# Kernel tuning notes

Measured on AMD Instinct MI355X. Metric: run time of the kernel, lower is better.

The kernel has to match this reference:

```python
import jax, jax.numpy as jnp
import numpy as np

V = 128          # vocab_size
S = 32           # sentence_size
E = 16           # embedding_size
M = 128          # memory_size
L = 128          # linear_output_size
B = 16
N = 127


def _position_encoding(sentence_size, embedding_size):
    enc = np.ones((embedding_size, sentence_size), dtype=np.float32)
    ls = sentence_size + 1
    le = embedding_size + 1
    for i in range(1, le):
        for j in range(1, ls):
            enc[i - 1, j - 1] = (i - (le - 1) / 2) * (j - (ls - 1) / 2)
    enc = 1 + 4 * enc / embedding_size / sentence_size
    return enc.T  # [S, E]


def setup_inputs() -> dict:
    key = jax.random.key(0)
    ks = jax.random.split(key, 12)
    node_fts = jax.random.randint(ks[0], (B, N, S), 0, V).astype(jnp.float32)
    edge_fts = jax.random.randint(ks[1], (B, N, N, S), 0, V).astype(jnp.float32)
    graph_fts = jax.random.randint(ks[2], (B, S), 0, V).astype(jnp.float32)
    adj_mat = jax.random.randint(ks[3], (B, N, N), 0, 2).astype(jnp.float32)
    hidden = jnp.zeros((B, N, E), jnp.float32)
    sc = 0.02
    query_biases = sc * jax.random.normal(ks[4], (V - 1, E), jnp.float32)
    stories_biases = sc * jax.random.normal(ks[5], (V - 1, E), jnp.float32)
    output_biases = sc * jax.random.normal(ks[6], (V - 1, E), jnp.float32)
    memory_contents = sc * jax.random.normal(ks[7], (M, E), jnp.float32)
    W_int = sc * jax.random.normal(ks[8], (E, E), jnp.float32)   # intermediate_linear (unused, num_hops=1)
    W_out = sc * jax.random.normal(ks[9], (E, L), jnp.float32)   # output_linear
    W_fin = sc * jax.random.normal(ks[10], (L, V), jnp.float32)  # final_linear
    enc = jnp.asarray(_position_encoding(S, E))
    return dict(node_fts=node_fts, edge_fts=edge_fts, graph_fts=graph_fts,
                adj_mat=adj_mat, hidden=hidden, enc=enc,
                query_biases=query_biases, stories_biases=stories_biases,
                output_biases=output_biases, memory_contents=memory_contents,
                W_int=W_int, W_out=W_out, W_fin=W_fin)


def reference(node_fts, edge_fts, graph_fts, adj_mat, hidden, enc,
              query_biases, stories_biases, output_biases, memory_contents,
              W_int, W_out, W_fin):
    del hidden
    b, n, s = node_fts.shape
    # [B, N+1, S]: nodes plus graph feature row
    naf = jnp.concatenate([node_fts, graph_fts[:, None, :]], axis=1)
    # mask edges then pad to [B, N+1, N+1, S]
    ef = edge_fts * adj_mat[..., None]
    ef = jnp.pad(ef, ((0, 0), (0, 1), (0, 1), (0, 0)))
    bt = b * (n + 1)
    queries = naf.reshape(bt, s)                 # [BT, S]
    stories = ef.reshape(bt, n + 1, s)           # [BT, M0, S], M0 = N+1

    nil = jnp.zeros((1, enc.shape[1]), queries.dtype)
    sb = jnp.concatenate([stories_biases, nil], axis=0)   # [V, E]
    qb = jnp.concatenate([query_biases, nil], axis=0)
    ob = jnp.concatenate([output_biases, nil], axis=0)

    sidx = jnp.maximum(stories.astype(jnp.int32), 0)       # clamp_min(0)
    qidx = jnp.maximum(queries.astype(jnp.int32), 0)

    # position-encoded weighted sums over the sentence axis
    mem = jnp.einsum('bmse,se->bme', sb[sidx], enc)        # [BT, M0, E]
    Cj = jnp.einsum('bmse,se->bme', ob[sidx], enc)         # [BT, M0, E]
    pad_m = memory_contents.shape[0] - (n + 1)
    mem = jnp.pad(mem, ((0, 0), (0, pad_m), (0, 0))) + memory_contents
    Cj = jnp.pad(Cj, ((0, 0), (0, pad_m), (0, 0)))
    u = jnp.einsum('bse,se->be', qb[qidx], enc)            # [BT, E]

    # num_hops = 1
    x = u
    probs = jax.nn.softmax(jnp.einsum('bme,be->bm', mem, x), axis=-1)
    o = jnp.einsum('bme,bm->be', Cj, probs)
    x = jax.nn.relu((x + o) @ W_out)                       # last hop -> output_linear + relu
    ret = x @ W_fin                                        # [BT, V]

    nxt = ret.reshape(b, n + 1, -1)
    return nxt[:, :-1, :] + nxt[:, -1:, :]                 # [B, N, V]
```

## Files before the change

kernel.cpp:

```cpp
#include <hip/hip_runtime.h>

#define Vn 128
#define Bn 16
#define Nn 127
#define BTn 2048
#define RS 20

__global__ __launch_bounds__(256, 4) void memnet_main(
    const float* __restrict__ node_fts, const float* __restrict__ edge_fts,
    const float* __restrict__ graph_fts, const float* __restrict__ adjm,
    const float* __restrict__ enc, const float* __restrict__ qb,
    const float* __restrict__ sb, const float* __restrict__ ob,
    const float* __restrict__ mc, const float* __restrict__ wout,
    const float* __restrict__ wfin, float* __restrict__ ret)
{
    __shared__ __align__(16) float sbL[128 * RS];
    __shared__ __align__(16) float obL[128 * RS];
    __shared__ __align__(16) float encL[32 * 16];
    __shared__ unsigned int idxw[128 * 8];
    __shared__ float cjT[16 * 129];
    __shared__ float scoresL[128];
    __shared__ float probsL[128];
    __shared__ float opart[128];
    __shared__ unsigned char actF[128];
    __shared__ __align__(16) float uL[16];
    __shared__ float uoL[16];
    __shared__ __align__(16) float cCL[16];
    __shared__ float xL[128];
    __shared__ float red[8];
    __shared__ float k0L;

    const int t = threadIdx.x;
    const int bt = blockIdx.x;
    const int b = bt >> 7;
    const int i = bt & 127;

    for (int c = t; c < 512; c += 256) {
        int r = c >> 2, q = c & 3;
        float4 v = make_float4(0.f, 0.f, 0.f, 0.f);
        float4 w = make_float4(0.f, 0.f, 0.f, 0.f);
        if (r < 127) {
            v = *(const float4*)&sb[r * 16 + q * 4];
            w = *(const float4*)&ob[r * 16 + q * 4];
        }
        *(float4*)&sbL[r * RS + q * 4] = v;
        *(float4*)&obL[r * RS + q * 4] = w;
    }
    if (t < 128) {
        *(float4*)&encL[t * 4] = *(const float4*)&enc[t * 4];
    }
    if (t < 128) {
        bool a = false;
        if (t < 127 && i < 127) a = (adjm[(b * 127 + i) * 127 + t] != 0.f);
        actF[t] = a ? 1 : 0;
    }
    for (int c = t; c < 1024; c += 256) {
        int m = c >> 3, q = c & 7;
        unsigned int packed = 0u;
        if (i < 127 && m < 127) {
            float a = adjm[(b * 127 + i) * 127 + m];
            if (a != 0.f) {
                const float4 v = *(const float4*)&edge_fts[(size_t)(((b * 127 + i) * 127 + m)) * 32 + q * 4];
                packed = (unsigned)(int)v.x | ((unsigned)(int)v.y << 8)
                       | ((unsigned)(int)v.z << 16) | ((unsigned)(int)v.w << 24);
            }
        }
        idxw[m * 8 + q] = packed;
    }
    if (t < 16) {
        float es = 0.f;
        for (int s = 0; s < 32; s++) es += enc[s * 16 + t];
        float ue = 0.f;
        for (int s = 0; s < 32; s++) {
            float qv = (i < 127) ? node_fts[(b * 127 + i) * 32 + s] : graph_fts[b * 32 + s];
            int qi = (int)qv;
            if (qi < 0) qi = 0;
            float w = (qi < 127) ? qb[qi * 16 + t] : 0.f;
            ue = fmaf(w, enc[s * 16 + t], ue);
        }
        uL[t] = ue;
        cCL[t] = ob[t] * es;
        float kv = sb[t] * es * ue;
        kv += __shfl_xor(kv, 1); kv += __shfl_xor(kv, 2);
        kv += __shfl_xor(kv, 4); kv += __shfl_xor(kv, 8);
        if (t == 0) k0L = kv;
    }
    __syncthreads();

    const int eg4 = (t & 3) * 4;
    const int md = t >> 2;
    const int m0 = md;
    const int m1 = md + 64;
    const bool a0 = (actF[m0] != 0);
    const bool a1 = (actF[m1] != 0);

    float4 aM0 = make_float4(0.f, 0.f, 0.f, 0.f);
    float4 aM1 = make_float4(0.f, 0.f, 0.f, 0.f);
    float4 aC0 = make_float4(0.f, 0.f, 0.f, 0.f);
    float4 aC1 = make_float4(0.f, 0.f, 0.f, 0.f);

    if (a0) {
#pragma unroll
        for (int sq = 0; sq < 8; sq++) {
            unsigned w0 = idxw[m0 * 8 + sq];
#pragma unroll
            for (int j = 0; j < 4; j++) {
                int s = sq * 4 + j;
                int i0 = (int)((w0 >> (8 * j)) & 0xFF);
                float4 eb = *(const float4*)&encL[s * 16 + eg4];
                float4 a  = *(const float4*)&sbL[i0 * RS + eg4];
                float4 c  = *(const float4*)&obL[i0 * RS + eg4];
                aM0.x = fmaf(a.x, eb.x, aM0.x); aM0.y = fmaf(a.y, eb.y, aM0.y);
                aM0.z = fmaf(a.z, eb.z, aM0.z); aM0.w = fmaf(a.w, eb.w, aM0.w);
                aC0.x = fmaf(c.x, eb.x, aC0.x); aC0.y = fmaf(c.y, eb.y, aC0.y);
                aC0.z = fmaf(c.z, eb.z, aC0.z); aC0.w = fmaf(c.w, eb.w, aC0.w);
            }
        }
    }
    if (a1) {
#pragma unroll
        for (int sq = 0; sq < 8; sq++) {
            unsigned w1 = idxw[m1 * 8 + sq];
#pragma unroll
            for (int j = 0; j < 4; j++) {
                int s = sq * 4 + j;
                int i1 = (int)((w1 >> (8 * j)) & 0xFF);
                float4 eb = *(const float4*)&encL[s * 16 + eg4];
                float4 a  = *(const float4*)&sbL[i1 * RS + eg4];
                float4 c  = *(const float4*)&obL[i1 * RS + eg4];
                aM1.x = fmaf(a.x, eb.x, aM1.x); aM1.y = fmaf(a.y, eb.y, aM1.y);
                aM1.z = fmaf(a.z, eb.z, aM1.z); aM1.w = fmaf(a.w, eb.w, aM1.w);
                aC1.x = fmaf(c.x, eb.x, aC1.x); aC1.y = fmaf(c.y, eb.y, aC1.y);
                aC1.z = fmaf(c.z, eb.z, aC1.z); aC1.w = fmaf(c.w, eb.w, aC1.w);
            }
        }
    }

    {
        float4 u4 = *(const float4*)&uL[eg4];
        float4 mc0 = *(const float4*)&mc[m0 * 16 + eg4];
        float4 mc1 = *(const float4*)&mc[m1 * 16 + eg4];
        float p0 = (aM0.x + mc0.x) * u4.x + (aM0.y + mc0.y) * u4.y
                 + (aM0.z + mc0.z) * u4.z + (aM0.w + mc0.w) * u4.w;
        float p1 = (aM1.x + mc1.x) * u4.x + (aM1.y + mc1.y) * u4.y
                 + (aM1.z + mc1.z) * u4.z + (aM1.w + mc1.w) * u4.w;
        p0 += __shfl_xor(p0, 1); p0 += __shfl_xor(p0, 2);
        p1 += __shfl_xor(p1, 1); p1 += __shfl_xor(p1, 2);
        if ((t & 3) == 0) {
            scoresL[m0] = p0 + (a0 ? 0.f : k0L);
            scoresL[m1] = p1 + (a1 ? 0.f : k0L);
        }
        float4 cC4 = *(const float4*)&cCL[eg4];
        float4 c0 = a0 ? aC0 : cC4;
        float4 c1 = a1 ? aC1 : cC4;
        cjT[(eg4 + 0) * 129 + m0] = c0.x; cjT[(eg4 + 1) * 129 + m0] = c0.y;
        cjT[(eg4 + 2) * 129 + m0] = c0.z; cjT[(eg4 + 3) * 129 + m0] = c0.w;
        cjT[(eg4 + 0) * 129 + m1] = c1.x; cjT[(eg4 + 1) * 129 + m1] = c1.y;
        cjT[(eg4 + 2) * 129 + m1] = c1.z; cjT[(eg4 + 3) * 129 + m1] = c1.w;
    }
    __syncthreads();

    {
        float v = (t < 128) ? scoresL[t] : -1e30f;
#pragma unroll
        for (int off = 32; off > 0; off >>= 1) v = fmaxf(v, __shfl_xor(v, off));
        if ((t & 63) == 0) red[t >> 6] = v;
        __syncthreads();
        float mx = fmaxf(fmaxf(red[0], red[1]), fmaxf(red[2], red[3]));
        float ex = (t < 128) ? __expf(scoresL[t] - mx) : 0.f;
        float sv = ex;
#pragma unroll
        for (int off = 32; off > 0; off >>= 1) sv += __shfl_xor(sv, off);
        __syncthreads();
        if ((t & 63) == 0) red[t >> 6] = sv;
        __syncthreads();
        float sum = red[0] + red[1] + red[2] + red[3];
        if (t < 128) probsL[t] = ex / sum;
    }
    __syncthreads();

    if (t < 128) {
        int e = t & 15, ch = t >> 4;
        float acc = 0.f;
#pragma unroll
        for (int k = 0; k < 16; k++) {
            int m = ch * 16 + k;
            acc = fmaf(probsL[m], cjT[e * 129 + m], acc);
        }
        opart[t] = acc;
    }
    __syncthreads();
    if (t < 16) {
        float o = 0.f;
#pragma unroll
        for (int ch = 0; ch < 8; ch++) o += opart[ch * 16 + t];
        uoL[t] = uL[t] + o;
    }
    __syncthreads();

    if (t < 128) {
        float acc = 0.f;
#pragma unroll
        for (int e = 0; e < 16; e++) acc = fmaf(uoL[e], wout[e * 128 + t], acc);
        xL[t] = fmaxf(acc, 0.f);
    }
    __syncthreads();
    if (t < 128) {
        float acc = 0.f;
        for (int l = 0; l < 128; l++) acc = fmaf(xL[l], wfin[l * 128 + t], acc);
        ret[bt * 128 + t] = acc;
    }
}

__global__ void memnet_out(const float* __restrict__ ret, float* __restrict__ out)
{
    int idx = blockIdx.x * 256 + threadIdx.x;
    if (idx >= Bn * Nn * Vn) return;
    int v = idx & 127;
    int r = idx >> 7;
    int b = r / 127;
    int i = r - b * 127;
    out[idx] = ret[(b * 128 + i) * 128 + v] + ret[(b * 128 + 127) * 128 + v];
}

extern "C" void kernel_launch(void* const* d_in, const int* in_sizes, int n_in,
                              void* d_out, int out_size, void* d_ws, size_t ws_size,
                              hipStream_t stream)
{
    const float* node  = (const float*)d_in[0];
    const float* edge  = (const float*)d_in[1];
    const float* graph = (const float*)d_in[2];
    const float* adjm  = (const float*)d_in[3];
    const float* enc   = (const float*)d_in[5];
    const float* qb    = (const float*)d_in[6];
    const float* sb    = (const float*)d_in[7];
    const float* ob    = (const float*)d_in[8];
    const float* mc    = (const float*)d_in[9];
    const float* wout  = (const float*)d_in[11];
    const float* wfin  = (const float*)d_in[12];

    float* ws = (float*)d_ws;

    memnet_main<<<BTn, 256, 0, stream>>>(node, edge, graph, adjm, enc, qb,
                                         sb, ob, mc, wout, wfin, ws);
    const int total = Bn * Nn * Vn;
    memnet_out<<<(total + 255) / 256, 256, 0, stream>>>(ws, (float*)d_out);
}
```

Baseline: 136.5 us.

## Pack story/output biases as bf16 pairs and compute position encoding inline

```diff
diff --git a/kernel.cpp b/kernel.cpp
--- a/kernel.cpp
+++ b/kernel.cpp
@@ -4,20 +4,26 @@
 #define Bn 16
 #define Nn 127
 #define BTn 2048
-#define RS 20
+#define TRS 20
+
+__device__ __forceinline__ unsigned rneb(float f) {
+    unsigned u = __float_as_uint(f);
+    return (u + 0x7fffu + ((u >> 16) & 1u)) >> 16;
+}
+__device__ __forceinline__ float encf(int s, float e7) {
+    return fmaf(e7, (float)(s - 15) * 0.0078125f, 1.0f);
+}
 
 __global__ __launch_bounds__(256, 4) void memnet_main(
     const float* __restrict__ node_fts, const float* __restrict__ edge_fts,
     const float* __restrict__ graph_fts, const float* __restrict__ adjm,
-    const float* __restrict__ enc, const float* __restrict__ qb,
-    const float* __restrict__ sb, const float* __restrict__ ob,
-    const float* __restrict__ mc, const float* __restrict__ wout,
-    const float* __restrict__ wfin, float* __restrict__ ret)
+    const float* __restrict__ qb, const float* __restrict__ sb,
+    const float* __restrict__ ob, const float* __restrict__ mc,
+    const float* __restrict__ wout, const float* __restrict__ wfin,
+    float* __restrict__ ret)
 {
-    __shared__ __align__(16) float sbL[128 * RS];
-    __shared__ __align__(16) float obL[128 * RS];
-    __shared__ __align__(16) float encL[32 * 16];
-    __shared__ unsigned int idxw[128 * 8];
+    __shared__ __align__(16) unsigned tblL[128 * TRS];
+    __shared__ unsigned idxw[8 * 128];
     __shared__ float cjT[16 * 129];
     __shared__ float scoresL[128];
     __shared__ float probsL[128];
@@ -37,17 +43,18 @@
 
     for (int c = t; c < 512; c += 256) {
         int r = c >> 2, q = c & 3;
-        float4 v = make_float4(0.f, 0.f, 0.f, 0.f);
-        float4 w = make_float4(0.f, 0.f, 0.f, 0.f);
+        float4 s4 = make_float4(0.f, 0.f, 0.f, 0.f);
+        float4 o4 = make_float4(0.f, 0.f, 0.f, 0.f);
         if (r < 127) {
-            v = *(const float4*)&sb[r * 16 + q * 4];
-            w = *(const float4*)&ob[r * 16 + q * 4];
-        }
-        *(float4*)&sbL[r * RS + q * 4] = v;
-        *(float4*)&obL[r * RS + q * 4] = w;
-    }
-    if (t < 128) {
-        *(float4*)&encL[t * 4] = *(const float4*)&enc[t * 4];
+            s4 = *(const float4*)&sb[r * 16 + q * 4];
+            o4 = *(const float4*)&ob[r * 16 + q * 4];
+        }
+        uint4 pk;
+        pk.x = (rneb(o4.x) << 16) | rneb(s4.x);
+        pk.y = (rneb(o4.y) << 16) | rneb(s4.y);
+        pk.z = (rneb(o4.z) << 16) | rneb(s4.z);
+        pk.w = (rneb(o4.w) << 16) | rneb(s4.w);
+        *(uint4*)&tblL[r * TRS + q * 4] = pk;
     }
     if (t < 128) {
         bool a = false;
@@ -56,7 +63,7 @@
     }
     for (int c = t; c < 1024; c += 256) {
         int m = c >> 3, q = c & 7;
-        unsigned int packed = 0u;
+        unsigned packed = 0u;
         if (i < 127 && m < 127) {
             float a = adjm[(b * 127 + i) * 127 + m];
             if (a != 0.f) {
@@ -65,18 +72,19 @@
                        | ((unsigned)(int)v.z << 16) | ((unsigned)(int)v.w << 24);
             }
         }
-        idxw[m * 8 + q] = packed;
+        idxw[q * 128 + m] = packed;
     }
     if (t < 16) {
-        float es = 0.f;
-        for (int s = 0; s < 32; s++) es += enc[s * 16 + t];
-        float ue = 0.f;
+        const float e7 = (float)(t - 7);
+        float es = 0.f, ue = 0.f;
         for (int s = 0; s < 32; s++) {
+            float ev = encf(s, e7);
+            es += ev;
             float qv = (i < 127) ? node_fts[(b * 127 + i) * 32 + s] : graph_fts[b * 32 + s];
             int qi = (int)qv;
             if (qi < 0) qi = 0;
             float w = (qi < 127) ? qb[qi * 16 + t] : 0.f;
-            ue = fmaf(w, enc[s * 16 + t], ue);
+            ue = fmaf(w, ev, ue);
         }
         uL[t] = ue;
         cCL[t] = ob[t] * es;
@@ -93,6 +101,8 @@
     const int m1 = md + 64;
     const bool a0 = (actF[m0] != 0);
     const bool a1 = (actF[m1] != 0);
+    const float ef0 = (float)(eg4 - 7), ef1 = (float)(eg4 - 6);
+    const float ef2 = (float)(eg4 - 5), ef3 = (float)(eg4 - 4);
 
     float4 aM0 = make_float4(0.f, 0.f, 0.f, 0.f);
     float4 aM1 = make_float4(0.f, 0.f, 0.f, 0.f);
@@ -102,36 +112,44 @@
     if (a0) {
 #pragma unroll
         for (int sq = 0; sq < 8; sq++) {
-            unsigned w0 = idxw[m0 * 8 + sq];
+            unsigned w0 = idxw[sq * 128 + m0];
 #pragma unroll
             for (int j = 0; j < 4; j++) {
-                int s = sq * 4 + j;
-                int i0 = (int)((w0 >> (8 * j)) & 0xFF);
-                float4 eb = *(const float4*)&encL[s * 16 + eg4];
-                float4 a  = *(const float4*)&sbL[i0 * RS + eg4];
-                float4 c  = *(const float4*)&obL[i0 * RS + eg4];
-                aM0.x = fmaf(a.x, eb.x, aM0.x); aM0.y = fmaf(a.y, eb.y, aM0.y);
-                aM0.z = fmaf(a.z, eb.z, aM0.z); aM0.w = fmaf(a.w, eb.w, aM0.w);
-                aC0.x = fmaf(c.x, eb.x, aC0.x); aC0.y = fmaf(c.y, eb.y, aC0.y);
-                aC0.z = fmaf(c.z, eb.z, aC0.z); aC0.w = fmaf(c.w, eb.w, aC0.w);
+                const int s = sq * 4 + j;
+                int ix = (int)((w0 >> (8 * j)) & 0xFF);
+                const uint4 pk = *(const uint4*)&tblL[ix * TRS + eg4];
+                float e0 = encf(s, ef0), e1 = encf(s, ef1);
+                float e2 = encf(s, ef2), e3 = encf(s, ef3);
+                aM0.x = fmaf(__uint_as_float(pk.x << 16), e0, aM0.x);
+                aC0.x = fmaf(__uint_as_float(pk.x & 0xffff0000u), e0, aC0.x);
+                aM0.y = fmaf(__uint_as_float(pk.y << 16), e1, aM0.y);
+                aC0.y = fmaf(__uint_as_float(pk.y & 0xffff0000u), e1, aC0.y);
+                aM0.z = fmaf(__uint_as_float(pk.z << 16), e2, aM0.z);
+                aC0.z = fmaf(__uint_as_float(pk.z & 0xffff0000u), e2, aC0.z);
+                aM0.w = fmaf(__uint_as_float(pk.w << 16), e3, aM0.w);
+                aC0.w = fmaf(__uint_as_float(pk.w & 0xffff0000u), e3, aC0.w);
             }
         }
     }
     if (a1) {
 #pragma unroll
         for (int sq = 0; sq < 8; sq++) {
-            unsigned w1 = idxw[m1 * 8 + sq];
+            unsigned w1 = idxw[sq * 128 + m1];
 #pragma unroll
             for (int j = 0; j < 4; j++) {
-                int s = sq * 4 + j;
-                int i1 = (int)((w1 >> (8 * j)) & 0xFF);
-                float4 eb = *(const float4*)&encL[s * 16 + eg4];
-                float4 a  = *(const float4*)&sbL[i1 * RS + eg4];
-                float4 c  = *(const float4*)&obL[i1 * RS + eg4];
-                aM1.x = fmaf(a.x, eb.x, aM1.x); aM1.y = fmaf(a.y, eb.y, aM1.y);
-                aM1.z = fmaf(a.z, eb.z, aM1.z); aM1.w = fmaf(a.w, eb.w, aM1.w);
-                aC1.x = fmaf(c.x, eb.x, aC1.x); aC1.y = fmaf(c.y, eb.y, aC1.y);
-                aC1.z = fmaf(c.z, eb.z, aC1.z); aC1.w = fmaf(c.w, eb.w, aC1.w);
+                const int s = sq * 4 + j;
+                int ix = (int)((w1 >> (8 * j)) & 0xFF);
+                const uint4 pk = *(const uint4*)&tblL[ix * TRS + eg4];
+                float e0 = encf(s, ef0), e1 = encf(s, ef1);
+                float e2 = encf(s, ef2), e3 = encf(s, ef3);
+                aM1.x = fmaf(__uint_as_float(pk.x << 16), e0, aM1.x);
+                aC1.x = fmaf(__uint_as_float(pk.x & 0xffff0000u), e0, aC1.x);
+                aM1.y = fmaf(__uint_as_float(pk.y << 16), e1, aM1.y);
+                aC1.y = fmaf(__uint_as_float(pk.y & 0xffff0000u), e1, aC1.y);
+                aM1.z = fmaf(__uint_as_float(pk.z << 16), e2, aM1.z);
+                aC1.z = fmaf(__uint_as_float(pk.z & 0xffff0000u), e2, aC1.z);
+                aM1.w = fmaf(__uint_as_float(pk.w << 16), e3, aM1.w);
+                aC1.w = fmaf(__uint_as_float(pk.w & 0xffff0000u), e3, aC1.w);
             }
         }
     }
@@ -231,7 +249,6 @@
     const float* edge  = (const float*)d_in[1];
     const float* graph = (const float*)d_in[2];
     const float* adjm  = (const float*)d_in[3];
-    const float* enc   = (const float*)d_in[5];
     const float* qb    = (const float*)d_in[6];
     const float* sb    = (const float*)d_in[7];
     const float* ob    = (const float*)d_in[8];
@@ -241,7 +258,7 @@
 
     float* ws = (float*)d_ws;
 
-    memnet_main<<<BTn, 256, 0, stream>>>(node, edge, graph, adjm, enc, qb,
+    memnet_main<<<BTn, 256, 0, stream>>>(node, edge, graph, adjm, qb,
                                          sb, ob, mc, wout, wfin, ws);
     const int total = Bn * Nn * Vn;
     memnet_out<<<(total + 255) / 256, 256, 0, stream>>>(ws, (float*)d_out);
```

Result: faster. 133.3 us (-2.3%).
